# Kernel optimization log

Measured on AMD Instinct MI355X. Metric: run time of the kernel, lower is better.

The kernel has to match this reference:

```python
import jax, jax.numpy as jnp
import numpy as np
from jax import lax

T, B, DIM, H, OUT = 512, 128, 512, 1024, 512


def setup_inputs() -> dict:
    key = jax.random.key(0)
    ks = jax.random.split(key, 7)
    s = lambda fan_in: 1.0 / np.sqrt(fan_in)
    return {
        "x": jax.random.normal(ks[0], (T, B, DIM), dtype=jnp.float32),
        "h0": jnp.zeros((B, H), dtype=jnp.float32),
        "Wx_w": jax.random.uniform(ks[1], (H, DIM), jnp.float32, -s(DIM), s(DIM)),
        "Wx_b": jax.random.uniform(ks[2], (H,), jnp.float32, -s(DIM), s(DIM)),
        "Wh_w": jax.random.uniform(ks[3], (H, H), jnp.float32, -s(H), s(H)),
        "Wh_b": jax.random.uniform(ks[4], (H,), jnp.float32, -s(H), s(H)),
        "Wo_w": jax.random.uniform(ks[5], (OUT, H), jnp.float32, -s(H), s(H)),
        "Wo_b": jax.random.uniform(ks[6], (OUT,), jnp.float32, -s(H), s(H)),
    }


def reference(x, h0, Wx_w, Wx_b, Wh_w, Wh_b, Wo_w, Wo_b):
    # Precompute the input projection for all timesteps in one big GEMM:
    # [T,B,DIM] @ [DIM,H] -> [T,B,H]  (Wx(x_t) + bias, includes Wh bias fused)
    xproj = jnp.einsum("tbd,hd->tbh", x, Wx_w) + Wx_b + Wh_b

    def step(h, xp_t):
        # h_{t} = tanh(Wh h_{t-1} + Wx x_t + biases)
        h_new = jnp.tanh(h @ Wh_w.T + xp_t)
        return h_new, h_new

    h_last, hs = lax.scan(step, h0, xproj)  # hs: [T,B,H]
    all_h = jnp.concatenate([h0[None], hs], axis=0)  # [T+1,B,H]
    # decode: F(Wo h_t) with F = sigmoid, batched over all steps
    all_y = jax.nn.sigmoid(jnp.einsum("tbh,oh->tbo", hs, Wo_w) + Wo_b)
    last_logits = h_last @ Wo_w.T + Wo_b  # Wo(all_h[-1]) without F
    return all_h, all_y, last_logits
```

## Files before the change

kernel.cpp:

```cpp
#include <hip/hip_runtime.h>
#include <hip/hip_bf16.h>

static constexpr int T_ = 512, B_ = 128, DIM_ = 512, H_ = 1024, OUT_ = 512;
static constexpr size_t BH = (size_t)B_ * H_;
static constexpr size_t HH = (size_t)H_ * H_;

using short8 = __attribute__((ext_vector_type(8))) short;
using f32x4  = __attribute__((ext_vector_type(4))) float;

__device__ __forceinline__ unsigned short f32_to_bf16(float x) {
    unsigned int u = __float_as_uint(x);
    u += 0x7fffu + ((u >> 16) & 1u);
    return (unsigned short)(u >> 16);
}
__device__ __forceinline__ float bf16_to_f32(unsigned short h) {
    return __uint_as_float(((unsigned int)h) << 16);
}

__global__ void copy_h0_kernel(const float* __restrict__ h0, float* __restrict__ out) {
    int i = blockIdx.x * blockDim.x + threadIdx.x;
    if (i < B_ * H_) out[i] = h0[i];
}

__global__ void cvt_planes_kernel(const float* __restrict__ src,
                                  unsigned short* __restrict__ hi,
                                  unsigned short* __restrict__ lo, int n4)
{
    int i = blockIdx.x * blockDim.x + threadIdx.x;
    if (i >= n4) return;
    const float4 v = *(const float4*)(src + (size_t)i * 4);
    unsigned short h[4] = {f32_to_bf16(v.x), f32_to_bf16(v.y),
                           f32_to_bf16(v.z), f32_to_bf16(v.w)};
    unsigned short l[4] = {f32_to_bf16(v.x - bf16_to_f32(h[0])),
                           f32_to_bf16(v.y - bf16_to_f32(h[1])),
                           f32_to_bf16(v.z - bf16_to_f32(h[2])),
                           f32_to_bf16(v.w - bf16_to_f32(h[3]))};
    *(ushort4*)(hi + (size_t)i * 4) = make_ushort4(h[0], h[1], h[2], h[3]);
    *(ushort4*)(lo + (size_t)i * 4) = make_ushort4(l[0], l[1], l[2], l[3]);
}

__global__ void pack_plane_kernel(const float* __restrict__ src,
                                  unsigned int* __restrict__ q, int n)
{
    int i = blockIdx.x * blockDim.x + threadIdx.x;
    if (i >= n) return;
    const float v = src[i];
    const unsigned short hi = f32_to_bf16(v);
    const unsigned short lo = f32_to_bf16(v - bf16_to_f32(hi));
    q[i] = (unsigned int)hi | ((unsigned int)lo << 16);
}

template<int SPLIT, int NB, int ACT>
__launch_bounds__(256)
__global__ void mfma_gemm(const float* __restrict__ A, const float* __restrict__ W,
                          const float* __restrict__ b1, const float* __restrict__ b2,
                          float* __restrict__ outp, int M, int N, int K)
{
    __shared__ unsigned short Ahi[128 * 32], Alo[SPLIT ? 128 * 32 : 1];
    __shared__ unsigned short Bhi[128 * 32], Blo[SPLIT ? 128 * 32 : 1];

    const int tid  = threadIdx.x;
    const int col0 = blockIdx.x * 128;
    const int row0 = blockIdx.y * 128;

    const int wv   = tid >> 6;
    const int lane = tid & 63;
    const int wr   = (wv >> 1) * 64;
    const int wc   = (wv & 1) * 64;

    f32x4 acc[4][4];
    #pragma unroll
    for (int i = 0; i < 4; ++i)
        #pragma unroll
        for (int j = 0; j < 4; ++j) acc[i][j] = (f32x4){0.f, 0.f, 0.f, 0.f};

    auto frag_off = [](int row, int unit) -> int {
        return row * 32 + ((unit ^ ((row >> 1) & 3)) << 3);
    };

    for (int k0 = 0; k0 < K; k0 += 32) {
        __syncthreads();
        #pragma unroll
        for (int i = 0; i < 4; ++i) {
            const int fid = tid + i * 256;
            const int row = fid >> 3;
            const int f4  = fid & 7;
            const int unit = f4 >> 1;
            const int uoff = ((unit ^ ((row >> 1) & 3)) << 3) + (f4 & 1) * 4;

            float4 av = *(const float4*)(A + (size_t)(row0 + row) * K + k0 + f4 * 4);
            float4 wvv = *(const float4*)(W + (size_t)(col0 + row) * K + k0 + f4 * 4);

            unsigned short ah[4] = {f32_to_bf16(av.x), f32_to_bf16(av.y),
                                    f32_to_bf16(av.z), f32_to_bf16(av.w)};
            unsigned short bh[4] = {f32_to_bf16(wvv.x), f32_to_bf16(wvv.y),
                                    f32_to_bf16(wvv.z), f32_to_bf16(wvv.w)};
            *(ushort4*)&Ahi[row * 32 + uoff] = make_ushort4(ah[0], ah[1], ah[2], ah[3]);
            *(ushort4*)&Bhi[row * 32 + uoff] = make_ushort4(bh[0], bh[1], bh[2], bh[3]);

            if constexpr (SPLIT) {
                unsigned short al[4] = {
                    f32_to_bf16(av.x - bf16_to_f32(ah[0])),
                    f32_to_bf16(av.y - bf16_to_f32(ah[1])),
                    f32_to_bf16(av.z - bf16_to_f32(ah[2])),
                    f32_to_bf16(av.w - bf16_to_f32(ah[3]))};
                unsigned short bl[4] = {
                    f32_to_bf16(wvv.x - bf16_to_f32(bh[0])),
                    f32_to_bf16(wvv.y - bf16_to_f32(bh[1])),
                    f32_to_bf16(wvv.z - bf16_to_f32(bh[2])),
                    f32_to_bf16(wvv.w - bf16_to_f32(bh[3]))};
                *(ushort4*)&Alo[row * 32 + uoff] = make_ushort4(al[0], al[1], al[2], al[3]);
                *(ushort4*)&Blo[row * 32 + uoff] = make_ushort4(bl[0], bl[1], bl[2], bl[3]);
            }
        }
        __syncthreads();

        const int lrow = lane & 15;
        const int unit = lane >> 4;

        short8 bh_f[4], bl_f[4];
        #pragma unroll
        for (int fc = 0; fc < 4; ++fc) {
            bh_f[fc] = *(const short8*)&Bhi[frag_off(wc + fc * 16 + lrow, unit)];
            if constexpr (SPLIT)
                bl_f[fc] = *(const short8*)&Blo[frag_off(wc + fc * 16 + lrow, unit)];
        }
        #pragma unroll
        for (int fr = 0; fr < 4; ++fr) {
            const short8 ah_f = *(const short8*)&Ahi[frag_off(wr + fr * 16 + lrow, unit)];
            if constexpr (SPLIT) {
                const short8 al_f = *(const short8*)&Alo[frag_off(wr + fr * 16 + lrow, unit)];
                #pragma unroll
                for (int fc = 0; fc < 4; ++fc) {
                    acc[fr][fc] = __builtin_amdgcn_mfma_f32_16x16x32_bf16(ah_f, bh_f[fc], acc[fr][fc], 0, 0, 0);
                    acc[fr][fc] = __builtin_amdgcn_mfma_f32_16x16x32_bf16(ah_f, bl_f[fc], acc[fr][fc], 0, 0, 0);
                    acc[fr][fc] = __builtin_amdgcn_mfma_f32_16x16x32_bf16(al_f, bh_f[fc], acc[fr][fc], 0, 0, 0);
                }
            } else {
                #pragma unroll
                for (int fc = 0; fc < 4; ++fc)
                    acc[fr][fc] = __builtin_amdgcn_mfma_f32_16x16x32_bf16(ah_f, bh_f[fc], acc[fr][fc], 0, 0, 0);
            }
        }
    }

    const int ccol = lane & 15;
    const int crow = (lane >> 4) * 4;
    #pragma unroll
    for (int fr = 0; fr < 4; ++fr) {
        #pragma unroll
        for (int fc = 0; fc < 4; ++fc) {
            const int col = col0 + wc + fc * 16 + ccol;
            float bias = 0.f;
            if constexpr (NB >= 1) bias += b1[col];
            if constexpr (NB >= 2) bias += b2[col];
            #pragma unroll
            for (int j = 0; j < 4; ++j) {
                const int row = row0 + wr + fr * 16 + crow + j;
                float v = acc[fr][fc][j] + bias;
                if constexpr (ACT == 1) v = tanhf(v);
                else if constexpr (ACT == 2) v = 1.0f / (1.0f + expf(-v));
                outp[(size_t)row * N + col] = v;
            }
        }
    }
}

__global__ __launch_bounds__(512, 1)
void rnn_persistent(const unsigned int* __restrict__ Ppk,
                    const unsigned short* __restrict__ Whi,
                    const unsigned short* __restrict__ Wlo,
                    float* __restrict__ all_h,
                    unsigned int* __restrict__ flags)
{
    __shared__ float red[8][16][33];

    const int tid  = threadIdx.x;
    const int bid  = blockIdx.x;
    const int y    = bid >> 5;
    const int x    = bid & 31;
    const int r0   = y * 16;
    const int c0   = x * 32;

    const int w    = tid >> 6;
    const int lane = tid & 63;
    const int lr   = lane & 15;
    const int kg   = lane >> 4;

    const int ep_r = tid >> 5, ep_c = tid & 31;
    const size_t ep_idx = (size_t)(r0 + ep_r) * H_ + (c0 + ep_c);

    const int kbase = w * 128 + kg * 8;
    const unsigned short* pb0h = Whi + (size_t)(c0 + lr) * H_ + kbase;
    const unsigned short* pb0l = Wlo + (size_t)(c0 + lr) * H_ + kbase;
    const unsigned short* pb1h = Whi + (size_t)(c0 + 16 + lr) * H_ + kbase;
    const unsigned short* pb1l = Wlo + (size_t)(c0 + 16 + lr) * H_ + kbase;

    short8 wb0h[4], wb0l[4], wb1h[4], wb1l[4];
    #pragma unroll
    for (int it = 0; it < 4; ++it) {
        const int ko = it * 32;
        wb0h[it] = *(const short8*)(pb0h + ko);
        wb0l[it] = *(const short8*)(pb0l + ko);
        wb1h[it] = *(const short8*)(pb1h + ko);
        wb1l[it] = *(const short8*)(pb1l + ko);
    }

    for (int t = 0; t < T_; ++t) {
        float* __restrict__ hdst = all_h + (size_t)(t + 1) * BH;
        const float xpv = hdst[ep_idx];

        const unsigned int* abase = Ppk + (size_t)(t & 1) * BH
                                  + (size_t)(r0 + lr) * H_ + kbase;
        uint4 c0v, c1v, c2v, c3v, c4v, c5v, c6v, c7v;
        asm volatile(
            "global_load_dwordx4 %0, %8, off sc0 sc1\n\t"
            "global_load_dwordx4 %1, %8, off offset:16 sc0 sc1\n\t"
            "global_load_dwordx4 %2, %8, off offset:128 sc0 sc1\n\t"
            "global_load_dwordx4 %3, %8, off offset:144 sc0 sc1\n\t"
            "global_load_dwordx4 %4, %8, off offset:256 sc0 sc1\n\t"
            "global_load_dwordx4 %5, %8, off offset:272 sc0 sc1\n\t"
            "global_load_dwordx4 %6, %8, off offset:384 sc0 sc1\n\t"
            "global_load_dwordx4 %7, %8, off offset:400 sc0 sc1\n\t"
            "s_waitcnt vmcnt(0)"
            : "=&v"(c0v), "=&v"(c1v), "=&v"(c2v), "=&v"(c3v),
              "=&v"(c4v), "=&v"(c5v), "=&v"(c6v), "=&v"(c7v)
            : "v"(abase)
            : "memory");

        f32x4 acc0 = {0.f, 0.f, 0.f, 0.f}, acc1 = {0.f, 0.f, 0.f, 0.f};
        const uint4 chunks[8] = {c0v, c1v, c2v, c3v, c4v, c5v, c6v, c7v};

        #pragma unroll
        for (int it = 0; it < 4; ++it) {
            short8 ah, al;
            #pragma unroll
            for (int j = 0; j < 4; ++j) {
                const unsigned int u0 = ((const unsigned int*)&chunks[2 * it])[j];
                const unsigned int u1 = ((const unsigned int*)&chunks[2 * it + 1])[j];
                ah[j]     = (short)(u0 & 0xffffu);
                al[j]     = (short)(u0 >> 16);
                ah[4 + j] = (short)(u1 & 0xffffu);
                al[4 + j] = (short)(u1 >> 16);
            }
            acc0 = __builtin_amdgcn_mfma_f32_16x16x32_bf16(ah, wb0h[it], acc0, 0, 0, 0);
            acc0 = __builtin_amdgcn_mfma_f32_16x16x32_bf16(ah, wb0l[it], acc0, 0, 0, 0);
            acc0 = __builtin_amdgcn_mfma_f32_16x16x32_bf16(al, wb0h[it], acc0, 0, 0, 0);
            acc0 = __builtin_amdgcn_mfma_f32_16x16x32_bf16(al, wb0l[it], acc0, 0, 0, 0);
            acc1 = __builtin_amdgcn_mfma_f32_16x16x32_bf16(ah, wb1h[it], acc1, 0, 0, 0);
            acc1 = __builtin_amdgcn_mfma_f32_16x16x32_bf16(ah, wb1l[it], acc1, 0, 0, 0);
            acc1 = __builtin_amdgcn_mfma_f32_16x16x32_bf16(al, wb1h[it], acc1, 0, 0, 0);
            acc1 = __builtin_amdgcn_mfma_f32_16x16x32_bf16(al, wb1l[it], acc1, 0, 0, 0);
        }

        #pragma unroll
        for (int j = 0; j < 4; ++j) {
            red[w][kg * 4 + j][lr]      = acc0[j];
            red[w][kg * 4 + j][16 + lr] = acc1[j];
        }
        __syncthreads();

        {
            float s = ((red[0][ep_r][ep_c] + red[1][ep_r][ep_c])
                     + (red[2][ep_r][ep_c] + red[3][ep_r][ep_c]))
                    + ((red[4][ep_r][ep_c] + red[5][ep_r][ep_c])
                     + (red[6][ep_r][ep_c] + red[7][ep_r][ep_c]));
            const float v = tanhf(s + xpv);
            hdst[ep_idx] = v;
            const unsigned short hi = f32_to_bf16(v);
            const unsigned short lo = f32_to_bf16(v - bf16_to_f32(hi));
            const unsigned int pk = (unsigned int)hi | ((unsigned int)lo << 16);
            const unsigned int* qp = Ppk + (size_t)((t + 1) & 1) * BH + ep_idx;
            asm volatile("global_store_dword %0, %1, off sc0 sc1"
                         :: "v"(qp), "v"(pk) : "memory");
        }

        asm volatile("s_waitcnt vmcnt(0)" ::: "memory");
        __syncthreads();
        if (tid == 0) {
            const unsigned int* fp = flags + bid;
            const unsigned int val = (unsigned int)(t + 1);
            asm volatile("global_store_dword %0, %1, off sc0 sc1\n\t"
                         "s_waitcnt vmcnt(0)"
                         :: "v"(fp), "v"(val) : "memory");
        }
        if (w == 0) {
            const unsigned int want = (unsigned int)(t + 1);
            const unsigned int* fp = flags + y * 32 + (lane & 31);
            unsigned int v = 0;
            int spins = 0;
            do {
                asm volatile("global_load_dword %0, %1, off sc0 sc1\n\t"
                             "s_waitcnt vmcnt(0)"
                             : "=v"(v) : "v"(fp) : "memory");
                if (v >= want) break_hint: ;
                if (++spins > (1 << 17)) break;
                if (v < want) __builtin_amdgcn_s_sleep(2);
            } while (!__all(v >= want));
        }
        __syncthreads();
    }
}

__global__ __launch_bounds__(512)
void step_v4(const unsigned short* __restrict__ Phi, const unsigned short* __restrict__ Plo,
             const unsigned short* __restrict__ Whi, const unsigned short* __restrict__ Wlo,
             float* __restrict__ hdst,
             unsigned short* __restrict__ Qhi, unsigned short* __restrict__ Qlo)
{
    __shared__ float red[8][16][33];

    const int tid  = threadIdx.x;
    const int c0   = blockIdx.x * 32;
    const int r0   = blockIdx.y * 16;
    const int w    = tid >> 6;
    const int lane = tid & 63;
    const int lr   = lane & 15;
    const int kg   = lane >> 4;

    const int ep_r = tid >> 5, ep_c = tid & 31;
    const size_t ep_idx = (size_t)(r0 + ep_r) * H_ + (c0 + ep_c);
    const float xpv = hdst[ep_idx];

    const int kbase = w * 128 + kg * 8;
    const unsigned short* pah = Phi + (size_t)(r0 + lr) * H_ + kbase;
    const unsigned short* pal = Plo + (size_t)(r0 + lr) * H_ + kbase;
    const unsigned short* pb0h = Whi + (size_t)(c0 + lr) * H_ + kbase;
    const unsigned short* pb0l = Wlo + (size_t)(c0 + lr) * H_ + kbase;
    const unsigned short* pb1h = Whi + (size_t)(c0 + 16 + lr) * H_ + kbase;
    const unsigned short* pb1l = Wlo + (size_t)(c0 + 16 + lr) * H_ + kbase;

    f32x4 acc0 = {0.f, 0.f, 0.f, 0.f}, acc1 = {0.f, 0.f, 0.f, 0.f};

    #pragma unroll
    for (int it = 0; it < 4; ++it) {
        const int ko = it * 32;
        const short8 ah  = *(const short8*)(pah + ko);
        const short8 al  = *(const short8*)(pal + ko);
        const short8 b0h = *(const short8*)(pb0h + ko);
        const short8 b0l = *(const short8*)(pb0l + ko);
        const short8 b1h = *(const short8*)(pb1h + ko);
        const short8 b1l = *(const short8*)(pb1l + ko);

        acc0 = __builtin_amdgcn_mfma_f32_16x16x32_bf16(ah, b0h, acc0, 0, 0, 0);
        acc0 = __builtin_amdgcn_mfma_f32_16x16x32_bf16(ah, b0l, acc0, 0, 0, 0);
        acc0 = __builtin_amdgcn_mfma_f32_16x16x32_bf16(al, b0h, acc0, 0, 0, 0);
        acc0 = __builtin_amdgcn_mfma_f32_16x16x32_bf16(al, b0l, acc0, 0, 0, 0);
        acc1 = __builtin_amdgcn_mfma_f32_16x16x32_bf16(ah, b1h, acc1, 0, 0, 0);
        acc1 = __builtin_amdgcn_mfma_f32_16x16x32_bf16(ah, b1l, acc1, 0, 0, 0);
        acc1 = __builtin_amdgcn_mfma_f32_16x16x32_bf16(al, b1h, acc1, 0, 0, 0);
        acc1 = __builtin_amdgcn_mfma_f32_16x16x32_bf16(al, b1l, acc1, 0, 0, 0);
    }

    #pragma unroll
    for (int j = 0; j < 4; ++j) {
        red[w][kg * 4 + j][lr]      = acc0[j];
        red[w][kg * 4 + j][16 + lr] = acc1[j];
    }
    __syncthreads();

    float s = ((red[0][ep_r][ep_c] + red[1][ep_r][ep_c])
             + (red[2][ep_r][ep_c] + red[3][ep_r][ep_c]))
            + ((red[4][ep_r][ep_c] + red[5][ep_r][ep_c])
             + (red[6][ep_r][ep_c] + red[7][ep_r][ep_c]));
    const float v = tanhf(s + xpv);
    hdst[ep_idx] = v;
    const unsigned short hi = f32_to_bf16(v);
    Qhi[ep_idx] = hi;
    Qlo[ep_idx] = f32_to_bf16(v - bf16_to_f32(hi));
}

__global__ __launch_bounds__(512)
void step_v3(const float* __restrict__ hsrc, const float* __restrict__ Wh,
             float* __restrict__ hdst)
{
    __shared__ float hS[16][1024];
    __shared__ float red[16][33];

    const int tid = threadIdx.x;
    const int c0  = blockIdx.x * 32;
    const int r0  = blockIdx.y * 16;

    const int ep_r = tid >> 5, ep_c = tid & 31;
    const size_t ep_idx = (size_t)(r0 + ep_r) * H_ + (c0 + ep_c);
    const float xpv = hdst[ep_idx];

    #pragma unroll
    for (int it = 0; it < 8; ++it) {
        const int chunk = tid + it * 512;
        const int row = chunk >> 8;
        const int k4  = (chunk & 255) * 4;
        *(float4*)&hS[row][k4] =
            *(const float4*)(hsrc + (size_t)(r0 + row) * H_ + k4);
    }
    __syncthreads();

    const int w     = tid >> 6;
    const int lane  = tid & 63;
    const int kslot = lane & 15;
    const int rq    = lane >> 4;

    float acc[4][4];
    #pragma unroll
    for (int r = 0; r < 4; ++r)
        #pragma unroll
        for (int c = 0; c < 4; ++c) acc[r][c] = 0.f;

    const float* whb = Wh + (size_t)(c0 + w * 4) * H_ + kslot * 4;

    #pragma unroll 4
    for (int i = 0; i < 16; ++i) {
        const int k = kslot * 4 + i * 64;
        float4 hv[4];
        #pragma unroll
        for (int r = 0; r < 4; ++r)
            hv[r] = *(const float4*)&hS[rq * 4 + r][k];
        #pragma unroll
        for (int c = 0; c < 4; ++c) {
            const float4 wvv = *(const float4*)(whb + (size_t)c * H_ + i * 64);
            #pragma unroll
            for (int r = 0; r < 4; ++r) {
                acc[r][c] = fmaf(hv[r].x, wvv.x, acc[r][c]);
                acc[r][c] = fmaf(hv[r].y, wvv.y, acc[r][c]);
                acc[r][c] = fmaf(hv[r].z, wvv.z, acc[r][c]);
                acc[r][c] = fmaf(hv[r].w, wvv.w, acc[r][c]);
            }
        }
    }

    #pragma unroll
    for (int m = 1; m < 16; m <<= 1)
        #pragma unroll
        for (int r = 0; r < 4; ++r)
            #pragma unroll
            for (int c = 0; c < 4; ++c)
                acc[r][c] += __shfl_xor(acc[r][c], m, 64);

    if (kslot == 0) {
        #pragma unroll
        for (int r = 0; r < 4; ++r)
            #pragma unroll
            for (int c = 0; c < 4; ++c)
                red[rq * 4 + r][w * 4 + c] = acc[r][c];
    }
    __syncthreads();

    hdst[ep_idx] = tanhf(red[ep_r][ep_c] + xpv);
}

extern "C" void kernel_launch(void* const* d_in, const int* in_sizes, int n_in,
                              void* d_out, int out_size, void* d_ws, size_t ws_size,
                              hipStream_t stream)
{
    const float* x    = (const float*)d_in[0];
    const float* h0   = (const float*)d_in[1];
    const float* Wx_w = (const float*)d_in[2];
    const float* Wx_b = (const float*)d_in[3];
    const float* Wh_w = (const float*)d_in[4];
    const float* Wh_b = (const float*)d_in[5];
    const float* Wo_w = (const float*)d_in[6];
    const float* Wo_b = (const float*)d_in[7];

    float* out   = (float*)d_out;
    float* all_h = out;
    float* all_y = out + (size_t)(T_ + 1) * BH;
    float* last  = all_y + (size_t)T_ * B_ * OUT_;

    copy_h0_kernel<<<dim3((B_*H_ + 255)/256), dim3(256), 0, stream>>>(h0, all_h);

    mfma_gemm<1, 2, 0><<<dim3(H_/128, (T_*B_)/128), dim3(256), 0, stream>>>(
        x, Wx_w, Wx_b, Wh_b, all_h + BH, T_*B_, H_, DIM_);

    const size_t need_pers = 2 * HH * sizeof(unsigned short)
                           + (2 * BH + 256) * sizeof(unsigned int);
    const size_t need_v4   = (2 * HH + 4 * BH) * sizeof(unsigned short);

    if (ws_size >= need_pers) {
        unsigned short* Whi = (unsigned short*)d_ws;
        unsigned short* Wlo = Whi + HH;
        unsigned int*   Ppk = (unsigned int*)(Whi + 2 * HH);
        unsigned int*   flg = Ppk + 2 * BH;

        cvt_planes_kernel<<<dim3((int)(HH/4/256)), dim3(256), 0, stream>>>(
            Wh_w, Whi, Wlo, (int)(HH/4));
        pack_plane_kernel<<<dim3((int)(BH/256)), dim3(256), 0, stream>>>(
            h0, Ppk, (int)BH);
        hipMemsetAsync(flg, 0, 256 * sizeof(unsigned int), stream);

        rnn_persistent<<<dim3(256), dim3(512), 0, stream>>>(
            Ppk, Whi, Wlo, all_h, flg);
    } else if (ws_size >= need_v4) {
        unsigned short* wsu = (unsigned short*)d_ws;
        unsigned short* Whi = wsu;
        unsigned short* Wlo = wsu + HH;
        unsigned short* P0h = wsu + 2 * HH;
        unsigned short* P0l = P0h + BH;
        unsigned short* P1h = P0l + BH;
        unsigned short* P1l = P1h + BH;

        cvt_planes_kernel<<<dim3((int)(HH/4/256)), dim3(256), 0, stream>>>(
            Wh_w, Whi, Wlo, (int)(HH/4));
        cvt_planes_kernel<<<dim3((int)(BH/4/256)), dim3(256), 0, stream>>>(
            h0, P0h, P0l, (int)(BH/4));

        for (int t = 0; t < T_; ++t) {
            unsigned short* ph = (t & 1) ? P1h : P0h;
            unsigned short* pl = (t & 1) ? P1l : P0l;
            unsigned short* qh = (t & 1) ? P0h : P1h;
            unsigned short* ql = (t & 1) ? P0l : P1l;
            step_v4<<<dim3(32, 8), dim3(512), 0, stream>>>(
                ph, pl, Whi, Wlo, all_h + (size_t)(t + 1) * BH, qh, ql);
        }
    } else {
        for (int t = 0; t < T_; ++t) {
            step_v3<<<dim3(32, 8), dim3(512), 0, stream>>>(
                all_h + (size_t)t * BH, Wh_w, all_h + (size_t)(t + 1) * BH);
        }
    }

    mfma_gemm<0, 1, 2><<<dim3(OUT_/128, (T_*B_)/128), dim3(256), 0, stream>>>(
        all_h + BH, Wo_w, Wo_b, nullptr, all_y, T_*B_, OUT_, H_);

    mfma_gemm<0, 1, 0><<<dim3(OUT_/128, 1), dim3(256), 0, stream>>>(
        all_h + (size_t)T_ * BH, Wo_w, Wo_b, nullptr, last, B_, OUT_, H_);
}
```

Before: 3.135 ms.

## Replace per-step flag barrier with sentinel-tagged triple-buffered hidden state

```diff
diff --git a/kernel.cpp b/kernel.cpp
--- a/kernel.cpp
+++ b/kernel.cpp
@@ -4,6 +4,7 @@
 static constexpr int T_ = 512, B_ = 128, DIM_ = 512, H_ = 1024, OUT_ = 512;
 static constexpr size_t BH = (size_t)B_ * H_;
 static constexpr size_t HH = (size_t)H_ * H_;
+static constexpr unsigned int SENT = 0xFFFFFFFFu;
 
 using short8 = __attribute__((ext_vector_type(8))) short;
 using f32x4  = __attribute__((ext_vector_type(4))) float;
@@ -167,11 +168,10 @@
 }
 
 __global__ __launch_bounds__(512, 1)
-void rnn_persistent(const unsigned int* __restrict__ Ppk,
+void rnn_persistent(unsigned int* __restrict__ Ppk,
                     const unsigned short* __restrict__ Whi,
                     const unsigned short* __restrict__ Wlo,
-                    float* __restrict__ all_h,
-                    unsigned int* __restrict__ flags)
+                    float* __restrict__ all_h)
 {
     __shared__ float red[8][16][33];
 
@@ -191,42 +191,57 @@
     const size_t ep_idx = (size_t)(r0 + ep_r) * H_ + (c0 + ep_c);
 
     const int kbase = w * 128 + kg * 8;
-    const unsigned short* pb0h = Whi + (size_t)(c0 + lr) * H_ + kbase;
-    const unsigned short* pb0l = Wlo + (size_t)(c0 + lr) * H_ + kbase;
-    const unsigned short* pb1h = Whi + (size_t)(c0 + 16 + lr) * H_ + kbase;
-    const unsigned short* pb1l = Wlo + (size_t)(c0 + 16 + lr) * H_ + kbase;
-
     short8 wb0h[4], wb0l[4], wb1h[4], wb1l[4];
     #pragma unroll
     for (int it = 0; it < 4; ++it) {
         const int ko = it * 32;
-        wb0h[it] = *(const short8*)(pb0h + ko);
-        wb0l[it] = *(const short8*)(pb0l + ko);
-        wb1h[it] = *(const short8*)(pb1h + ko);
-        wb1l[it] = *(const short8*)(pb1l + ko);
-    }
+        wb0h[it] = *(const short8*)(Whi + (size_t)(c0 + lr) * H_ + kbase + ko);
+        wb0l[it] = *(const short8*)(Wlo + (size_t)(c0 + lr) * H_ + kbase + ko);
+        wb1h[it] = *(const short8*)(Whi + (size_t)(c0 + 16 + lr) * H_ + kbase + ko);
+        wb1l[it] = *(const short8*)(Wlo + (size_t)(c0 + 16 + lr) * H_ + kbase + ko);
+    }
+
+    const size_t arow = (size_t)(r0 + lr) * H_ + kbase;
 
     for (int t = 0; t < T_; ++t) {
         float* __restrict__ hdst = all_h + (size_t)(t + 1) * BH;
         const float xpv = hdst[ep_idx];
 
-        const unsigned int* abase = Ppk + (size_t)(t & 1) * BH
-                                  + (size_t)(r0 + lr) * H_ + kbase;
+        const unsigned int* abase = Ppk + (size_t)(t % 3) * BH + arow;
         uint4 c0v, c1v, c2v, c3v, c4v, c5v, c6v, c7v;
-        asm volatile(
-            "global_load_dwordx4 %0, %8, off sc0 sc1\n\t"
-            "global_load_dwordx4 %1, %8, off offset:16 sc0 sc1\n\t"
-            "global_load_dwordx4 %2, %8, off offset:128 sc0 sc1\n\t"
-            "global_load_dwordx4 %3, %8, off offset:144 sc0 sc1\n\t"
-            "global_load_dwordx4 %4, %8, off offset:256 sc0 sc1\n\t"
-            "global_load_dwordx4 %5, %8, off offset:272 sc0 sc1\n\t"
-            "global_load_dwordx4 %6, %8, off offset:384 sc0 sc1\n\t"
-            "global_load_dwordx4 %7, %8, off offset:400 sc0 sc1\n\t"
-            "s_waitcnt vmcnt(0)"
-            : "=&v"(c0v), "=&v"(c1v), "=&v"(c2v), "=&v"(c3v),
-              "=&v"(c4v), "=&v"(c5v), "=&v"(c6v), "=&v"(c7v)
-            : "v"(abase)
-            : "memory");
+        int spins = 0;
+        bool ok;
+        do {
+            asm volatile(
+                "global_load_dwordx4 %0, %8, off sc0 sc1\n\t"
+                "global_load_dwordx4 %1, %8, off offset:16 sc0 sc1\n\t"
+                "global_load_dwordx4 %2, %8, off offset:128 sc0 sc1\n\t"
+                "global_load_dwordx4 %3, %8, off offset:144 sc0 sc1\n\t"
+                "global_load_dwordx4 %4, %8, off offset:256 sc0 sc1\n\t"
+                "global_load_dwordx4 %5, %8, off offset:272 sc0 sc1\n\t"
+                "global_load_dwordx4 %6, %8, off offset:384 sc0 sc1\n\t"
+                "global_load_dwordx4 %7, %8, off offset:400 sc0 sc1\n\t"
+                "s_waitcnt vmcnt(0)"
+                : "=&v"(c0v), "=&v"(c1v), "=&v"(c2v), "=&v"(c3v),
+                  "=&v"(c4v), "=&v"(c5v), "=&v"(c6v), "=&v"(c7v)
+                : "v"(abase));
+            ok = true;
+            #define CHK(u) ok &= ((u).x != SENT) & ((u).y != SENT) & \
+                                 ((u).z != SENT) & ((u).w != SENT)
+            CHK(c0v); CHK(c1v); CHK(c2v); CHK(c3v);
+            CHK(c4v); CHK(c5v); CHK(c6v); CHK(c7v);
+            #undef CHK
+            if (__all(ok)) break;
+            if (++spins > (1 << 17)) break;
+            __builtin_amdgcn_s_sleep(1);
+        } while (true);
+
+        {
+            unsigned int* cp = Ppk + (size_t)((t + 2) % 3) * BH + ep_idx;
+            const unsigned int sv = SENT;
+            asm volatile("global_store_dword %0, %1, off sc0 sc1"
+                         :: "v"(cp), "v"(sv));
+        }
 
         f32x4 acc0 = {0.f, 0.f, 0.f, 0.f}, acc1 = {0.f, 0.f, 0.f, 0.f};
         const uint4 chunks[8] = {c0v, c1v, c2v, c3v, c4v, c5v, c6v, c7v};
@@ -270,33 +285,10 @@
             const unsigned short hi = f32_to_bf16(v);
             const unsigned short lo = f32_to_bf16(v - bf16_to_f32(hi));
             const unsigned int pk = (unsigned int)hi | ((unsigned int)lo << 16);
-            const unsigned int* qp = Ppk + (size_t)((t + 1) & 1) * BH + ep_idx;
-            asm volatile("global_store_dword %0, %1, off sc0 sc1"
-                         :: "v"(qp), "v"(pk) : "memory");
-        }
-
-        asm volatile("s_waitcnt vmcnt(0)" ::: "memory");
-        __syncthreads();
-        if (tid == 0) {
-            const unsigned int* fp = flags + bid;
-            const unsigned int val = (unsigned int)(t + 1);
-            asm volatile("global_store_dword %0, %1, off sc0 sc1\n\t"
-                         "s_waitcnt vmcnt(0)"
-                         :: "v"(fp), "v"(val) : "memory");
-        }
-        if (w == 0) {
-            const unsigned int want = (unsigned int)(t + 1);
-            const unsigned int* fp = flags + y * 32 + (lane & 31);
-            unsigned int v = 0;
-            int spins = 0;
-            do {
-                asm volatile("global_load_dword %0, %1, off sc0 sc1\n\t"
-                             "s_waitcnt vmcnt(0)"
-                             : "=v"(v) : "v"(fp) : "memory");
-                if (v >= want) break_hint: ;
-                if (++spins > (1 << 17)) break;
-                if (v < want) __builtin_amdgcn_s_sleep(2);
-            } while (!__all(v >= want));
+            unsigned int* qp = Ppk + (size_t)((t + 1) % 3) * BH + ep_idx;
+            asm volatile("s_waitcnt vmcnt(0)\n\t"
+                         "global_store_dword %0, %1, off sc0 sc1"
+                         :: "v"(qp), "v"(pk));
         }
         __syncthreads();
     }
@@ -370,84 +362,6 @@
     Qlo[ep_idx] = f32_to_bf16(v - bf16_to_f32(hi));
 }
 
-__global__ __launch_bounds__(512)
-void step_v3(const float* __restrict__ hsrc, const float* __restrict__ Wh,
-             float* __restrict__ hdst)
-{
-    __shared__ float hS[16][1024];
-    __shared__ float red[16][33];
-
-    const int tid = threadIdx.x;
-    const int c0  = blockIdx.x * 32;
-    const int r0  = blockIdx.y * 16;
-
-    const int ep_r = tid >> 5, ep_c = tid & 31;
-    const size_t ep_idx = (size_t)(r0 + ep_r) * H_ + (c0 + ep_c);
-    const float xpv = hdst[ep_idx];
-
-    #pragma unroll
-    for (int it = 0; it < 8; ++it) {
-        const int chunk = tid + it * 512;
-        const int row = chunk >> 8;
-        const int k4  = (chunk & 255) * 4;
-        *(float4*)&hS[row][k4] =
-            *(const float4*)(hsrc + (size_t)(r0 + row) * H_ + k4);
-    }
-    __syncthreads();
-
-    const int w     = tid >> 6;
-    const int lane  = tid & 63;
-    const int kslot = lane & 15;
-    const int rq    = lane >> 4;
-
-    float acc[4][4];
-    #pragma unroll
-    for (int r = 0; r < 4; ++r)
-        #pragma unroll
-        for (int c = 0; c < 4; ++c) acc[r][c] = 0.f;
-
-    const float* whb = Wh + (size_t)(c0 + w * 4) * H_ + kslot * 4;
-
-    #pragma unroll 4
-    for (int i = 0; i < 16; ++i) {
-        const int k = kslot * 4 + i * 64;
-        float4 hv[4];
-        #pragma unroll
-        for (int r = 0; r < 4; ++r)
-            hv[r] = *(const float4*)&hS[rq * 4 + r][k];
-        #pragma unroll
-        for (int c = 0; c < 4; ++c) {
-            const float4 wvv = *(const float4*)(whb + (size_t)c * H_ + i * 64);
-            #pragma unroll
-            for (int r = 0; r < 4; ++r) {
-                acc[r][c] = fmaf(hv[r].x, wvv.x, acc[r][c]);
-                acc[r][c] = fmaf(hv[r].y, wvv.y, acc[r][c]);
-                acc[r][c] = fmaf(hv[r].z, wvv.z, acc[r][c]);
-                acc[r][c] = fmaf(hv[r].w, wvv.w, acc[r][c]);
-            }
-        }
-    }
-
-    #pragma unroll
-    for (int m = 1; m < 16; m <<= 1)
-        #pragma unroll
-        for (int r = 0; r < 4; ++r)
-            #pragma unroll
-            for (int c = 0; c < 4; ++c)
-                acc[r][c] += __shfl_xor(acc[r][c], m, 64);
-
-    if (kslot == 0) {
-        #pragma unroll
-        for (int r = 0; r < 4; ++r)
-            #pragma unroll
-            for (int c = 0; c < 4; ++c)
-                red[rq * 4 + r][w * 4 + c] = acc[r][c];
-    }
-    __syncthreads();
-
-    hdst[ep_idx] = tanhf(red[ep_r][ep_c] + xpv);
-}
-
 extern "C" void kernel_launch(void* const* d_in, const int* in_sizes, int n_in,
                               void* d_out, int out_size, void* d_ws, size_t ws_size,
                               hipStream_t stream)
@@ -472,23 +386,22 @@
         x, Wx_w, Wx_b, Wh_b, all_h + BH, T_*B_, H_, DIM_);
 
     const size_t need_pers = 2 * HH * sizeof(unsigned short)
-                           + (2 * BH + 256) * sizeof(unsigned int);
+                           + 3 * BH * sizeof(unsigned int);
     const size_t need_v4   = (2 * HH + 4 * BH) * sizeof(unsigned short);
 
     if (ws_size >= need_pers) {
         unsigned short* Whi = (unsigned short*)d_ws;
         unsigned short* Wlo = Whi + HH;
         unsigned int*   Ppk = (unsigned int*)(Whi + 2 * HH);
-        unsigned int*   flg = Ppk + 2 * BH;
 
         cvt_planes_kernel<<<dim3((int)(HH/4/256)), dim3(256), 0, stream>>>(
             Wh_w, Whi, Wlo, (int)(HH/4));
         pack_plane_kernel<<<dim3((int)(BH/256)), dim3(256), 0, stream>>>(
             h0, Ppk, (int)BH);
-        hipMemsetAsync(flg, 0, 256 * sizeof(unsigned int), stream);
+        hipMemsetAsync(Ppk + BH, 0xFF, 2 * BH * sizeof(unsigned int), stream);
 
         rnn_persistent<<<dim3(256), dim3(512), 0, stream>>>(
-            Ppk, Whi, Wlo, all_h, flg);
+            Ppk, Whi, Wlo, all_h);
     } else if (ws_size >= need_v4) {
         unsigned short* wsu = (unsigned short*)d_ws;
         unsigned short* Whi = wsu;
@@ -511,11 +424,6 @@
             step_v4<<<dim3(32, 8), dim3(512), 0, stream>>>(
                 ph, pl, Whi, Wlo, all_h + (size_t)(t + 1) * BH, qh, ql);
         }
-    } else {
-        for (int t = 0; t < T_; ++t) {
-            step_v3<<<dim3(32, 8), dim3(512), 0, stream>>>(
-                all_h + (size_t)t * BH, Wh_w, all_h + (size_t)(t + 1) * BH);
-        }
     }
 
     mfma_gemm<0, 1, 2><<<dim3(OUT_/128, (T_*B_)/128), dim3(256), 0, stream>>>(
```

New measurement: 2.792 ms. -10.9%, faster.
